# Optimization experiments

Measured on AMD Instinct MI355X. Metric: run time of the kernel, lower is better.

Reference implementation:

```python
import jax, jax.numpy as jnp
import numpy as np

EPS = 1e-7
N_NODES = 100000

# --- Lorentz model (c = 1), working at the origin o = (1, 0, ..., 0) ---

def expmap0(v_spatial):
    """Exp map at origin: tangent spatial part [N, d] -> hyperboloid point [N, d+1]."""
    nrm = jnp.sqrt(jnp.maximum(jnp.sum(v_spatial * v_spatial, axis=-1, keepdims=True), EPS))
    x0 = jnp.cosh(nrm)
    xs = jnp.sinh(nrm) / nrm * v_spatial
    return jnp.concatenate([x0, xs], axis=-1)


def logmap0(x):
    """Log map at origin: point [N, d+1] -> tangent spatial part [N, d]."""
    x0 = jnp.maximum(x[..., :1], 1.0 + EPS)
    xs = x[..., 1:]
    nrm = jnp.sqrt(jnp.maximum(jnp.sum(xs * xs, axis=-1, keepdims=True), EPS))
    return jnp.arccosh(x0) / nrm * xs


def sigmoid_nonlin(x):
    # log map -> sigmoid in tangent space -> exp map (c_in = c_out = 1)
    return expmap0(jax.nn.sigmoid(logmap0(x)))


def hgcn_layer(x, edge_index, W, b):
    """HGCN conv: tangent-space linear + mean aggregation over edges + exp map."""
    t = logmap0(x)                      # [N, d_in]
    h = t @ W + b                       # [N, d_out]
    src, dst = edge_index[0], edge_index[1]
    msg = h[src]                        # [E, d_out] gather
    agg = jax.ops.segment_sum(msg, dst, num_segments=N_NODES)
    deg = jax.ops.segment_sum(jnp.ones((edge_index.shape[1],), h.dtype), dst,
                              num_segments=N_NODES)
    agg = agg / jnp.maximum(deg, 1.0)[:, None]
    return expmap0(agg)


def setup_inputs() -> dict:
    key = jax.random.key(0)
    ks = jax.random.split(key, 10)
    d_in, h1, h2, h_mlp, d_out = 64, 64, 64, 128, 40
    return {
        "features": jax.random.normal(ks[0], (N_NODES, d_in), jnp.float32),
        "edge_index": jax.random.randint(ks[1], (2, 1600000), 0, N_NODES, jnp.int64),
        "W1": jax.random.normal(ks[2], (d_in, h1), jnp.float32) * 0.05,
        "b1": jnp.zeros((h1,), jnp.float32),
        "W2": jax.random.normal(ks[3], (h1, h2), jnp.float32) * 0.05,
        "b2": jnp.zeros((h2,), jnp.float32),
        "W3": jax.random.normal(ks[4], (h2, h_mlp), jnp.float32) * 0.05,
        "b3": jnp.zeros((h_mlp,), jnp.float32),
        "W4": jax.random.normal(ks[5], (h_mlp, d_out), jnp.float32) * 0.05,
        "b4": jnp.zeros((d_out,), jnp.float32),
    }


def reference(features, edge_index, W1, b1, W2, b2, W3, b3, W4, b4):
    # lift Euclidean features to the hyperboloid (pad time coord, exp map)
    x = expmap0(features)                       # [N, d_in+1]
    x = hgcn_layer(x, edge_index, W1, b1)
    x = sigmoid_nonlin(x)
    x = hgcn_layer(x, edge_index, W2, b2)
    x = sigmoid_nonlin(x)
    t = logmap0(x)                              # [N, h2] (spatial part, drops time coord)
    # MLP head (dropout inactive at eval)
    h = jax.nn.relu(t @ W3 + b3)
    return h @ W4 + b4
```

## Files before the change

### kernel.cpp

```cpp
#include <hip/hip_runtime.h>


constexpr int CSHIFT = 9;
constexpr int CNODES = 1 << CSHIFT;
constexpr int EPB    = 4096;
constexpr int EPT    = EPB / 256;
constexpr int CAP    = 16384;

constexpr int W1F_OFF = 0;
constexpr int W2F_OFF = 4096;
constexpr int W3F_OFF = 8192;
constexpr int W4F_OFF = 16384;
constexpr int WIMG_TOT = 22528;

typedef __attribute__((ext_vector_type(8))) short short8;
typedef __attribute__((ext_vector_type(4))) float floatx4;

__device__ __forceinline__ float sigmoidf(float x) {
    return 1.0f / (1.0f + __expf(-x));
}
__device__ __forceinline__ unsigned short f2bf(float f) {
    unsigned int u = __float_as_uint(f);
    u = (u + 0x7FFFu + ((u >> 16) & 1u)) >> 16;
    return (unsigned short)u;
}

__global__ __launch_bounds__(256) void part_prep_k(
    const int* __restrict__ src, const int* __restrict__ dst,
    int* __restrict__ ccur, int* __restrict__ arena, int E, int NBUCK, int gP,
    const float* __restrict__ feat, unsigned short* __restrict__ featbf,
    const float* __restrict__ W1, const float* __restrict__ W2,
    const float* __restrict__ W3, const float* __restrict__ W4,
    unsigned short* __restrict__ img, int n8)
{
    __shared__ int  hist[256];
    __shared__ int  exoff[256];
    __shared__ int  lcur[256];
    __shared__ int  gbase[256];
    __shared__ int  stage[EPB];
    __shared__ unsigned char stageB[EPB];

    const int tid = threadIdx.x;

    if ((int)blockIdx.x >= gP) {
        int i = ((int)blockIdx.x - gP) * 256 + tid;
        if (i < n8) {
            const float4* p = (const float4*)feat + (size_t)i * 2;
            float4 a = p[0], b = p[1];
            uint4 o;
            o.x = (unsigned)f2bf(a.x) | ((unsigned)f2bf(a.y) << 16);
            o.y = (unsigned)f2bf(a.z) | ((unsigned)f2bf(a.w) << 16);
            o.z = (unsigned)f2bf(b.x) | ((unsigned)f2bf(b.y) << 16);
            o.w = (unsigned)f2bf(b.z) | ((unsigned)f2bf(b.w) << 16);
            ((uint4*)featbf)[i] = o;
            return;
        }
        int t = i - n8;
        if (t >= WIMG_TOT) return;
        float v = 0.f;
        int s = t;
        if (s < W2F_OFF) {
            int j = s & 7, m = (s >> 3) & 15, q = (s >> 7) & 3, kk = (s >> 9) & 1, c = s >> 10;
            v = W1[(kk * 32 + q * 8 + j) * 64 + c * 16 + m];
        } else if (s < W3F_OFF) {
            s -= W2F_OFF;
            int j = s & 7, m = (s >> 3) & 15, q = (s >> 7) & 3, kk = (s >> 9) & 1, c = s >> 10;
            v = W2[(kk * 32 + q * 8 + j) * 64 + c * 16 + m];
        } else if (s < W4F_OFF) {
            s -= W3F_OFF;
            int j = s & 7, m = (s >> 3) & 15, q = (s >> 7) & 3, kk = (s >> 9) & 1, c = s >> 10;
            v = W3[(kk * 32 + q * 8 + j) * 128 + c * 16 + m];
        } else {
            s -= W4F_OFF;
            int j = s & 7, m = (s >> 3) & 15, q = (s >> 7) & 3, kk = (s >> 9) & 3, c = s >> 11;
            int n = c * 16 + m;
            if (n < 40) v = W4[(kk * 32 + q * 8 + j) * 40 + n];
        }
        img[t] = f2bf(v);
        return;
    }

    const int e0  = blockIdx.x * EPB;
    const int ec  = min(EPB, E - e0);

    int pk[EPT], bk[EPT];
    hist[tid] = 0;
    __syncthreads();
    #pragma unroll
    for (int j = 0; j < EPT; j++) {
        int idx = tid + j * 256;
        if (idx < ec) {
            int s = src[e0 + idx];
            int d = dst[e0 + idx];
            bk[j] = d >> CSHIFT;
            pk[j] = s | ((d & (CNODES - 1)) << 17);
            atomicAdd(&hist[bk[j]], 1);
        } else bk[j] = -1;
    }
    __syncthreads();
    const int h = hist[tid];
    exoff[tid] = h;
    __syncthreads();
    for (int dd = 1; dd < 256; dd <<= 1) {
        int v = 0;
        if (tid >= dd) v = exoff[tid - dd];
        __syncthreads();
        if (tid >= dd) exoff[tid] += v;
        __syncthreads();
    }
    const int ex = exoff[tid] - h;
    int gb = 0;
    if (tid < NBUCK && h > 0) gb = atomicAdd(ccur + tid, h);
    __syncthreads();
    exoff[tid] = ex;
    lcur[tid]  = ex;
    gbase[tid] = gb;
    __syncthreads();
    #pragma unroll
    for (int j = 0; j < EPT; j++) {
        if (bk[j] >= 0) {
            int l = atomicAdd(&lcur[bk[j]], 1);
            stage[l]  = pk[j];
            stageB[l] = (unsigned char)bk[j];
        }
    }
    __syncthreads();
    for (int i = tid; i < ec; i += 256) {
        int b = stageB[i];
        arena[(size_t)b * CAP + gbase[b] + (i - exoff[b])] = stage[i];
    }
}

__global__ __launch_bounds__(256) void csr_fine(const int* __restrict__ arena,
                                                const int* __restrict__ ccur,
                                                int* __restrict__ off,
                                                int* __restrict__ ssrc,
                                                int N, int E, int NBUCK) {
    __shared__ int cnt[CNODES];
    __shared__ int cur[CNODES];
    __shared__ int part[256];
    const int b = blockIdx.x;
    const int node0 = b << CSHIFT;
    const int tid = threadIdx.x;

    part[tid] = (tid < NBUCK) ? ccur[tid] : 0;
    __syncthreads();
    for (int d = 1; d < 256; d <<= 1) {
        int v = 0;
        if (tid >= d) v = part[tid - d];
        __syncthreads();
        if (tid >= d) part[tid] += v;
        __syncthreads();
    }
    const int cbeg = (b > 0) ? part[b - 1] : 0;
    const int ec   = ccur[b];
    if (b == 0 && tid == 0) off[N] = E;
    __syncthreads();

    const int* pe = arena + (size_t)b * CAP;
    cnt[tid] = 0;
    cnt[tid + 256] = 0;
    __syncthreads();
    for (int i = tid; i < ec; i += 256)
        atomicAdd(&cnt[(pe[i] >> 17) & (CNODES - 1)], 1);
    __syncthreads();
    const int c0 = cnt[2 * tid], c1 = cnt[2 * tid + 1];
    part[tid] = c0 + c1;
    __syncthreads();
    for (int d = 1; d < 256; d <<= 1) {
        int v = 0;
        if (tid >= d) v = part[tid - d];
        __syncthreads();
        if (tid >= d) part[tid] += v;
        __syncthreads();
    }
    const int ex = (tid > 0) ? part[tid - 1] : 0;
    cur[2 * tid]     = ex;
    cur[2 * tid + 1] = ex + c0;
    if (node0 + 2 * tid     < N) off[node0 + 2 * tid]     = cbeg + ex;
    if (node0 + 2 * tid + 1 < N) off[node0 + 2 * tid + 1] = cbeg + ex + c0;
    __syncthreads();
    for (int i = tid; i < ec; i += 256) {
        int p = pe[i];
        int pos = cbeg + atomicAdd(&cur[(p >> 17) & (CNODES - 1)], 1);
        ssrc[pos] = p & 0x1FFFF;
    }
}

#define ACC8(v)                                    \
    acc[0] += __uint_as_float((v).x << 16);        \
    acc[1] += __uint_as_float((v).x & 0xFFFF0000u);\
    acc[2] += __uint_as_float((v).y << 16);        \
    acc[3] += __uint_as_float((v).y & 0xFFFF0000u);\
    acc[4] += __uint_as_float((v).z << 16);        \
    acc[5] += __uint_as_float((v).z & 0xFFFF0000u);\
    acc[6] += __uint_as_float((v).w << 16);        \
    acc[7] += __uint_as_float((v).w & 0xFFFF0000u);

__device__ __forceinline__ void gather_tile_wave(
    const unsigned short* __restrict__ h, const int* __restrict__ off,
    const int* __restrict__ ssrc, unsigned short* Agg, int rowB, int N,
    int w, int lane)
{
    #pragma unroll
    for (int pass = 0; pass < 2; pass++) {
        int rl = w * 16 + pass * 8 + (lane >> 3);
        int g  = rowB + rl;
        int q  = (lane & 7) * 8;
        uint4 p = make_uint4(0u, 0u, 0u, 0u);
        if (g < N) {
            int beg = off[g], end = off[g + 1];
            float acc[8] = {0.f, 0.f, 0.f, 0.f, 0.f, 0.f, 0.f, 0.f};
            int i = beg;
            for (; i + 8 <= end; i += 8) {
                uint4 v0 = *(const uint4*)(h + (size_t)ssrc[i]     * 64 + q);
                uint4 v1 = *(const uint4*)(h + (size_t)ssrc[i + 1] * 64 + q);
                uint4 v2 = *(const uint4*)(h + (size_t)ssrc[i + 2] * 64 + q);
                uint4 v3 = *(const uint4*)(h + (size_t)ssrc[i + 3] * 64 + q);
                uint4 v4 = *(const uint4*)(h + (size_t)ssrc[i + 4] * 64 + q);
                uint4 v5 = *(const uint4*)(h + (size_t)ssrc[i + 5] * 64 + q);
                uint4 v6 = *(const uint4*)(h + (size_t)ssrc[i + 6] * 64 + q);
                uint4 v7 = *(const uint4*)(h + (size_t)ssrc[i + 7] * 64 + q);
                ACC8(v0); ACC8(v1); ACC8(v2); ACC8(v3);
                ACC8(v4); ACC8(v5); ACC8(v6); ACC8(v7);
            }
            for (; i + 2 <= end; i += 2) {
                uint4 v0 = *(const uint4*)(h + (size_t)ssrc[i]     * 64 + q);
                uint4 v1 = *(const uint4*)(h + (size_t)ssrc[i + 1] * 64 + q);
                ACC8(v0); ACC8(v1);
            }
            for (; i < end; i++) {
                uint4 v = *(const uint4*)(h + (size_t)ssrc[i] * 64 + q);
                ACC8(v);
            }
            float inv = __builtin_amdgcn_rcpf((float)max(end - beg, 1));
            p.x = (unsigned)f2bf(acc[0]*inv) | ((unsigned)f2bf(acc[1]*inv) << 16);
            p.y = (unsigned)f2bf(acc[2]*inv) | ((unsigned)f2bf(acc[3]*inv) << 16);
            p.z = (unsigned)f2bf(acc[4]*inv) | ((unsigned)f2bf(acc[5]*inv) << 16);
            p.w = (unsigned)f2bf(acc[6]*inv) | ((unsigned)f2bf(acc[7]*inv) << 16);
        }
        *(uint4*)(Agg + rl * 72 + q) = p;
    }
}

__global__ __launch_bounds__(256) void aggemm1_k(
    const unsigned short* __restrict__ featbf, const int* __restrict__ off,
    const int* __restrict__ ssrc, const unsigned short* __restrict__ img,
    const float* __restrict__ bias, unsigned short* __restrict__ t1, int N)
{
    __shared__ alignas(16) unsigned short Agg[64 * 72];

    const int tid = threadIdx.x;
    const int rowB = blockIdx.x * 64;
    const int w = tid >> 6, lane = tid & 63;
    const int m = lane & 15, quad = lane >> 4;
    const int row0 = rowB + w * 16;

    gather_tile_wave(featbf, off, ssrc, Agg, rowB, N, w, lane);

    const short8* Wf = (const short8*)(img + W1F_OFF);
    floatx4 acc[4];
    #pragma unroll
    for (int c = 0; c < 4; c++) acc[c] = (floatx4){0.f, 0.f, 0.f, 0.f};
    #pragma unroll
    for (int kk = 0; kk < 2; kk++) {
        short8 a = *(const short8*)(Agg + (w * 16 + m) * 72 + kk * 32 + quad * 8);
        #pragma unroll
        for (int c = 0; c < 4; c++) {
            short8 b = Wf[((c * 2 + kk) * 4 + quad) * 16 + m];
            acc[c] = __builtin_amdgcn_mfma_f32_16x16x32_bf16(a, b, acc[c], 0, 0, 0);
        }
    }
    bool dzr[4];
    int rows[4];
    #pragma unroll
    for (int r = 0; r < 4; r++) {
        rows[r] = row0 + quad * 4 + r;
        dzr[r] = (rows[r] < N) ? (off[rows[r] + 1] == off[rows[r]]) : false;
    }
    #pragma unroll
    for (int c = 0; c < 4; c++) {
        int col = c * 16 + m;
        float bv = bias[col];
        #pragma unroll
        for (int r = 0; r < 4; r++) {
            if (rows[r] < N) {
                float v = dzr[r] ? 0.5f : sigmoidf(acc[c][r] + bv);
                t1[(size_t)rows[r] * 64 + col] = f2bf(v);
            }
        }
    }
}

__global__ __launch_bounds__(256) void aggep3_k(
    const unsigned short* __restrict__ t1, const int* __restrict__ off,
    const int* __restrict__ ssrc, const unsigned short* __restrict__ img,
    const float* __restrict__ b2, const float* __restrict__ b3,
    const float* __restrict__ b4, float* __restrict__ out, int N)
{
    __shared__ alignas(16) unsigned short SM[9216];
    unsigned short* T2  = SM;
    unsigned short* Agg = SM + 4608;
    unsigned short* H3h = SM + 4608;

    const int tid = threadIdx.x;
    const int rowB = blockIdx.x * 64;
    const int w = tid >> 6, lane = tid & 63;
    const int m = lane & 15, quad = lane >> 4;
    const int row0 = rowB + w * 16;

    gather_tile_wave(t1, off, ssrc, Agg, rowB, N, w, lane);

    {
        const short8* Wf = (const short8*)(img + W2F_OFF);
        floatx4 acc[4];
        #pragma unroll
        for (int c = 0; c < 4; c++) acc[c] = (floatx4){0.f, 0.f, 0.f, 0.f};
        #pragma unroll
        for (int kk = 0; kk < 2; kk++) {
            short8 a = *(const short8*)(Agg + (w * 16 + m) * 72 + kk * 32 + quad * 8);
            #pragma unroll
            for (int c = 0; c < 4; c++) {
                short8 b = Wf[((c * 2 + kk) * 4 + quad) * 16 + m];
                acc[c] = __builtin_amdgcn_mfma_f32_16x16x32_bf16(a, b, acc[c], 0, 0, 0);
            }
        }
        bool dzr[4];
        #pragma unroll
        for (int r = 0; r < 4; r++) {
            int row = row0 + quad * 4 + r;
            dzr[r] = (row < N) ? (off[row + 1] == off[row]) : false;
        }
        #pragma unroll
        for (int c = 0; c < 4; c++) {
            int col = c * 16 + m;
            float bv = b2[col];
            #pragma unroll
            for (int r = 0; r < 4; r++) {
                int rl = w * 16 + quad * 4 + r;
                float v = dzr[r] ? 0.5f : sigmoidf(acc[c][r] + bv);
                T2[rl * 72 + col] = f2bf(v);
            }
        }
    }

    floatx4 acc2[3];
    #pragma unroll
    for (int c = 0; c < 3; c++) acc2[c] = (floatx4){0.f, 0.f, 0.f, 0.f};
    const short8* Wf3 = (const short8*)(img + W3F_OFF);
    const short8* Wf4 = (const short8*)(img + W4F_OFF);

    #pragma unroll
    for (int half = 0; half < 2; half++) {
        floatx4 acc[4];
        #pragma unroll
        for (int c = 0; c < 4; c++) acc[c] = (floatx4){0.f, 0.f, 0.f, 0.f};
        #pragma unroll
        for (int kk = 0; kk < 2; kk++) {
            short8 a = *(const short8*)(T2 + (w * 16 + m) * 72 + kk * 32 + quad * 8);
            #pragma unroll
            for (int c = 0; c < 4; c++) {
                short8 b = Wf3[(((half * 4 + c) * 2 + kk) * 4 + quad) * 16 + m];
                acc[c] = __builtin_amdgcn_mfma_f32_16x16x32_bf16(a, b, acc[c], 0, 0, 0);
            }
        }
        #pragma unroll
        for (int c = 0; c < 4; c++) {
            int col = c * 16 + m;
            float bv = b3[half * 64 + col];
            #pragma unroll
            for (int r = 0; r < 4; r++) {
                int rl = w * 16 + quad * 4 + r;
                H3h[rl * 72 + col] = f2bf(fmaxf(acc[c][r] + bv, 0.f));
            }
        }
        #pragma unroll
        for (int kk2 = 0; kk2 < 2; kk2++) {
            short8 a = *(const short8*)(H3h + (w * 16 + m) * 72 + kk2 * 32 + quad * 8);
            #pragma unroll
            for (int c = 0; c < 3; c++) {
                short8 b = Wf4[((c * 4 + half * 2 + kk2) * 4 + quad) * 16 + m];
                acc2[c] = __builtin_amdgcn_mfma_f32_16x16x32_bf16(a, b, acc2[c], 0, 0, 0);
            }
        }
    }

    #pragma unroll
    for (int c = 0; c < 3; c++) {
        int col = c * 16 + m;
        if (col < 40) {
            float bv = b4[col];
            #pragma unroll
            for (int r = 0; r < 4; r++) {
                int row = row0 + quad * 4 + r;
                if (row < N) out[(size_t)row * 40 + col] = acc2[c][r] + bv;
            }
        }
    }
}

extern "C" void kernel_launch(void* const* d_in, const int* in_sizes, int n_in,
                              void* d_out, int out_size, void* d_ws, size_t ws_size,
                              hipStream_t stream)
{
    const float* feat = (const float*)d_in[0];
    const int*   eidx = (const int*)d_in[1];
    const float* W1 = (const float*)d_in[2];
    const float* b1 = (const float*)d_in[3];
    const float* W2 = (const float*)d_in[4];
    const float* b2 = (const float*)d_in[5];
    const float* W3 = (const float*)d_in[6];
    const float* b3 = (const float*)d_in[7];
    const float* W4 = (const float*)d_in[8];
    const float* b4 = (const float*)d_in[9];

    const int N = in_sizes[0] / 64;
    const int E = in_sizes[1] / 2;
    const int* src = eidx;
    const int* dst = eidx + E;

    const int NBUCK = (N + CNODES - 1) / CNODES;

    unsigned short* featbf = (unsigned short*)d_ws;
    unsigned short* t1     = featbf + (size_t)N * 64;
    unsigned short* img    = t1     + (size_t)N * 64;
    int*   off   = (int*)(img + WIMG_TOT);
    int*   ccur  = off + (N + 1);
    int*   ssrc  = ccur + NBUCK;
    int*   arena = ssrc + E;
    float* out   = (float*)d_out;

    hipMemsetAsync(ccur, 0, (size_t)NBUCK * sizeof(int), stream);

    const dim3 blk(256);
    const int gP  = (E + EPB - 1) / EPB;
    const int g64 = (N + 63) / 64;
    const int n8  = N * 64 / 8;
    const int gPC = (n8 + WIMG_TOT + 255) / 256;

    part_prep_k<<<gP + gPC, blk, 0, stream>>>(src, dst, ccur, arena, E, NBUCK,
                                              gP, feat, featbf, W1, W2, W3, W4,
                                              img, n8);
    csr_fine<<<NBUCK, blk, 0, stream>>>(arena, ccur, off, ssrc, N, E, NBUCK);

    aggemm1_k<<<g64, blk, 0, stream>>>(featbf, off, ssrc, img, b1, t1, N);
    aggep3_k<<<g64, blk, 0, stream>>>(t1, off, ssrc, img, b2, b3, b4, out, N);
}
```

Measured before the change: 229.4 us.

## Widen CSR bucket blocks to 1024 threads and halve aggregation tile rows

The fine CSR build now runs 1024 threads per bucket and replaces the two-nodes-per-thread shared-memory scan with a wave shuffle scan plus a small per-wave prefix, so each thread handles one node. The edge count is also clamped to CAP. The two gather+GEMM kernels now process 32 rows per 128-thread block instead of 64 rows per 256 threads. This doubles the grid size and halves LDS per block, aiming for better occupancy and load balance in the gather-heavy phases, at the cost of more blocks and more per-block overhead such as weight loads.

```diff
diff --git a/kernel.cpp b/kernel.cpp
--- a/kernel.cpp
+++ b/kernel.cpp
@@ -131,56 +131,63 @@
     }
 }
 
-__global__ __launch_bounds__(256) void csr_fine(const int* __restrict__ arena,
-                                                const int* __restrict__ ccur,
-                                                int* __restrict__ off,
-                                                int* __restrict__ ssrc,
-                                                int N, int E, int NBUCK) {
+__global__ __launch_bounds__(1024) void csr_fine(const int* __restrict__ arena,
+                                                 const int* __restrict__ ccur,
+                                                 int* __restrict__ off,
+                                                 int* __restrict__ ssrc,
+                                                 int N, int E, int NBUCK) {
+    __shared__ int part[256];
     __shared__ int cnt[CNODES];
     __shared__ int cur[CNODES];
-    __shared__ int part[256];
+    __shared__ int wpre[8];
     const int b = blockIdx.x;
     const int node0 = b << CSHIFT;
     const int tid = threadIdx.x;
-
-    part[tid] = (tid < NBUCK) ? ccur[tid] : 0;
+    const int lane = tid & 63, wid = tid >> 6;
+
+    if (tid < 256) part[tid] = (tid < NBUCK) ? ccur[tid] : 0;
     __syncthreads();
     for (int d = 1; d < 256; d <<= 1) {
         int v = 0;
-        if (tid >= d) v = part[tid - d];
+        if (tid < 256 && tid >= d) v = part[tid - d];
         __syncthreads();
-        if (tid >= d) part[tid] += v;
+        if (tid < 256 && tid >= d) part[tid] += v;
         __syncthreads();
     }
     const int cbeg = (b > 0) ? part[b - 1] : 0;
-    const int ec   = ccur[b];
+    const int ec   = min(ccur[b], CAP);
     if (b == 0 && tid == 0) off[N] = E;
-    __syncthreads();
-
+
+    if (tid < CNODES) cnt[tid] = 0;
+    __syncthreads();
     const int* pe = arena + (size_t)b * CAP;
-    cnt[tid] = 0;
-    cnt[tid + 256] = 0;
-    __syncthreads();
-    for (int i = tid; i < ec; i += 256)
+    for (int i = tid; i < ec; i += 1024)
         atomicAdd(&cnt[(pe[i] >> 17) & (CNODES - 1)], 1);
     __syncthreads();
-    const int c0 = cnt[2 * tid], c1 = cnt[2 * tid + 1];
-    part[tid] = c0 + c1;
-    __syncthreads();
-    for (int d = 1; d < 256; d <<= 1) {
-        int v = 0;
-        if (tid >= d) v = part[tid - d];
-        __syncthreads();
-        if (tid >= d) part[tid] += v;
-        __syncthreads();
-    }
-    const int ex = (tid > 0) ? part[tid - 1] : 0;
-    cur[2 * tid]     = ex;
-    cur[2 * tid + 1] = ex + c0;
-    if (node0 + 2 * tid     < N) off[node0 + 2 * tid]     = cbeg + ex;
-    if (node0 + 2 * tid + 1 < N) off[node0 + 2 * tid + 1] = cbeg + ex + c0;
-    __syncthreads();
-    for (int i = tid; i < ec; i += 256) {
+
+    int c = (tid < CNODES) ? cnt[tid] : 0;
+    int v = c;
+    #pragma unroll
+    for (int d = 1; d < 64; d <<= 1) {
+        int t = __shfl_up(v, d);
+        if (lane >= d) v += t;
+    }
+    if (tid < CNODES && lane == 63) wpre[wid] = v;
+    __syncthreads();
+    if (tid == 0) {
+        int s = 0;
+        #pragma unroll
+        for (int k = 0; k < CNODES / 64; k++) { int t = wpre[k]; wpre[k] = s; s += t; }
+    }
+    __syncthreads();
+    if (tid < CNODES) {
+        int ex = wpre[wid] + v - c;
+        cur[tid] = ex;
+        int node = node0 + tid;
+        if (node < N) off[node] = cbeg + ex;
+    }
+    __syncthreads();
+    for (int i = tid; i < ec; i += 1024) {
         int p = pe[i];
         int pos = cbeg + atomicAdd(&cur[(p >> 17) & (CNODES - 1)], 1);
         ssrc[pos] = p & 0x1FFFF;
@@ -243,15 +250,15 @@
     }
 }
 
-__global__ __launch_bounds__(256) void aggemm1_k(
+__global__ __launch_bounds__(128) void aggemm1_k(
     const unsigned short* __restrict__ featbf, const int* __restrict__ off,
     const int* __restrict__ ssrc, const unsigned short* __restrict__ img,
     const float* __restrict__ bias, unsigned short* __restrict__ t1, int N)
 {
-    __shared__ alignas(16) unsigned short Agg[64 * 72];
+    __shared__ alignas(16) unsigned short Agg[32 * 72];
 
     const int tid = threadIdx.x;
-    const int rowB = blockIdx.x * 64;
+    const int rowB = blockIdx.x * 32;
     const int w = tid >> 6, lane = tid & 63;
     const int m = lane & 15, quad = lane >> 4;
     const int row0 = rowB + w * 16;
@@ -292,19 +299,19 @@
     }
 }
 
-__global__ __launch_bounds__(256) void aggep3_k(
+__global__ __launch_bounds__(128) void aggep3_k(
     const unsigned short* __restrict__ t1, const int* __restrict__ off,
     const int* __restrict__ ssrc, const unsigned short* __restrict__ img,
     const float* __restrict__ b2, const float* __restrict__ b3,
     const float* __restrict__ b4, float* __restrict__ out, int N)
 {
-    __shared__ alignas(16) unsigned short SM[9216];
+    __shared__ alignas(16) unsigned short SM[4608];
     unsigned short* T2  = SM;
-    unsigned short* Agg = SM + 4608;
-    unsigned short* H3h = SM + 4608;
+    unsigned short* Agg = SM + 2304;
+    unsigned short* H3h = SM + 2304;
 
     const int tid = threadIdx.x;
-    const int rowB = blockIdx.x * 64;
+    const int rowB = blockIdx.x * 32;
     const int w = tid >> 6, lane = tid & 63;
     const int m = lane & 15, quad = lane >> 4;
     const int row0 = rowB + w * 16;
@@ -434,15 +441,15 @@
 
     const dim3 blk(256);
     const int gP  = (E + EPB - 1) / EPB;
-    const int g64 = (N + 63) / 64;
+    const int g32 = (N + 31) / 32;
     const int n8  = N * 64 / 8;
     const int gPC = (n8 + WIMG_TOT + 255) / 256;
 
     part_prep_k<<<gP + gPC, blk, 0, stream>>>(src, dst, ccur, arena, E, NBUCK,
                                               gP, feat, featbf, W1, W2, W3, W4,
                                               img, n8);
-    csr_fine<<<NBUCK, blk, 0, stream>>>(arena, ccur, off, ssrc, N, E, NBUCK);
-
-    aggemm1_k<<<g64, blk, 0, stream>>>(featbf, off, ssrc, img, b1, t1, N);
-    aggep3_k<<<g64, blk, 0, stream>>>(t1, off, ssrc, img, b2, b3, b4, out, N);
-}
+    csr_fine<<<NBUCK, dim3(1024), 0, stream>>>(arena, ccur, off, ssrc, N, E, NBUCK);
+
+    aggemm1_k<<<g32, dim3(128), 0, stream>>>(featbf, off, ssrc, img, b1, t1, N);
+    aggep3_k<<<g32, dim3(128), 0, stream>>>(t1, off, ssrc, img, b2, b3, b4, out, N);
+}
```

New measurement: 219.1 us. 1.05x faster.
